# Optimization experiments

Hardware: AMD Instinct MI355X
Metric: run time of the kernel (lower is better)

The kernel has to match this reference:

```python
import jax, jax.numpy as jnp
import numpy as np

GROUP_MANTISSA = 8
GROUP_SIZE = 36


def bfp_quantize(x, mantissa=GROUP_MANTISSA, group_size=GROUP_SIZE):
    """Block floating point: flatten, group consecutive group_size elements,
    share the max exponent within each group, keep `mantissa` mantissa bits."""
    flat = x.reshape(-1)
    n = flat.shape[0]
    pad = (-n) % group_size
    f = jnp.pad(flat, (0, pad)).reshape(-1, group_size)  # [G, group_size]
    m = jnp.max(jnp.abs(f), axis=1, keepdims=True)       # group max magnitude
    safe_m = jnp.where(m > 0, m, jnp.ones_like(m))
    e = jnp.floor(jnp.log2(safe_m))                      # shared exponent
    scale = jnp.exp2(e - (mantissa - 1))                 # LSB step for the group
    q = jnp.round(f / scale) * scale
    q = jnp.where(m > 0, q, jnp.zeros_like(q))
    return q.reshape(-1)[:n].reshape(x.shape)


def setup_inputs() -> dict:
    key = jax.random.key(0)
    kx, kw, kb = jax.random.split(key, 3)
    x = jax.random.normal(kx, (32, 64, 112, 112), dtype=jnp.float32)
    # kaiming-uniform-ish scale for a 3x3x64 fan-in
    fan_in = 64 * 3 * 3
    bound = 1.0 / np.sqrt(fan_in)
    weight = jax.random.uniform(kw, (64, 64, 3, 3), dtype=jnp.float32, minval=-bound, maxval=bound) * np.sqrt(3.0)
    bias = jax.random.uniform(kb, (64,), dtype=jnp.float32, minval=-bound, maxval=bound)
    return {"x": x, "weight": weight, "bias": bias}


def reference(x, weight, bias):
    xq = bfp_quantize(x)
    wq = bfp_quantize(weight)
    out = jax.lax.conv_general_dilated(
        xq, wq,
        window_strides=(1, 1),
        padding=((1, 1), (1, 1)),
        lhs_dilation=(1, 1),
        rhs_dilation=(1, 1),
        dimension_numbers=("NCHW", "OIHW", "NCHW"),
        feature_group_count=1,
    )
    return out + bias[None, :, None, None]
```

## Files before the change

### kernel.cpp

```cpp
#include <hip/hip_runtime.h>

typedef __attribute__((ext_vector_type(4))) float f32x4;
typedef __attribute__((ext_vector_type(8))) short s16x8;
typedef __attribute__((ext_vector_type(2))) unsigned int u32x2;
typedef __attribute__((ext_vector_type(4))) unsigned int u32x4;

#define X_ELEMS 25690112
#define X_F4    6422528
#define HW 112
#define CHW (64*112*112)

__device__ __forceinline__ unsigned short f32_to_bf16_exact(float q) {
    return (unsigned short)(__float_as_uint(q) >> 16);
}

__device__ __forceinline__ unsigned int pack_bf16x2(float a, float b) {
    return __builtin_amdgcn_perm(__float_as_uint(b), __float_as_uint(a), 0x07060302u);
}

__device__ __forceinline__ void scale_from_max(float m, float& scale, float& inv) {
    if (m > 0.f) {
        int e = (int)((__float_as_uint(m) >> 23) & 0xFF) - 127;
        scale = __builtin_ldexpf(1.0f, e - 7);
        inv   = __builtin_ldexpf(1.0f, 7 - e);
    } else { scale = 0.f; inv = 0.f; }
}

__global__ __launch_bounds__(256) void q1_quant(const float* __restrict__ x,
                                                const float* __restrict__ w,
                                                unsigned short* __restrict__ xq,
                                                unsigned short* __restrict__ wt) {
    __shared__ float lmax[2304];
    __shared__ float lsc[256];
    __shared__ float linv[256];
    const int b = blockIdx.x, tid = threadIdx.x;

    if (b == 2788) {
        #pragma unroll 1
        for (int rep = 0; rep < 4; ++rep) {
            int g = rep * 256 + tid;
            const float4* p = (const float4*)w + g * 9;
            float vv[36]; float m = 0.f;
            #pragma unroll
            for (int i = 0; i < 9; ++i) {
                float4 v = p[i];
                vv[i*4+0]=v.x; vv[i*4+1]=v.y; vv[i*4+2]=v.z; vv[i*4+3]=v.w;
                m = fmaxf(m, fmaxf(fmaxf(fabsf(v.x), fabsf(v.y)), fmaxf(fabsf(v.z), fabsf(v.w))));
            }
            float s, inv; scale_from_max(m, s, inv);
            #pragma unroll
            for (int j = 0; j < 36; ++j) {
                int flat = g * 36 + j;
                int k = flat / 576, rem = flat % 576;
                int c = rem / 9, pp = rem % 9;
                float q = rintf(vv[j] * inv) * s;
                wt[pp * 4096 + k * 64 + c] = f32_to_bf16_exact(q);
            }
        }
        return;
    }

    long base4 = (long)b * 2304;
    float4 vv[9];
    #pragma unroll
    for (int it = 0; it < 9; ++it) {
        int i = it * 256 + tid;
        long g4 = base4 + i;
        float4 v = {0.f, 0.f, 0.f, 0.f};
        if (g4 < X_F4) v = ((const float4*)x)[g4];
        vv[it] = v;
        lmax[i] = fmaxf(fmaxf(fabsf(v.x), fabsf(v.y)), fmaxf(fabsf(v.z), fabsf(v.w)));
    }
    __syncthreads();
    {
        float m = 0.f; int o = tid * 9;
        #pragma unroll
        for (int j = 0; j < 9; ++j) m = fmaxf(m, lmax[o + j]);
        float s, inv; scale_from_max(m, s, inv);
        lsc[tid] = s; linv[tid] = inv;
    }
    __syncthreads();
    #pragma unroll
    for (int it = 0; it < 9; ++it) {
        int i = it * 256 + tid;
        long g4 = base4 + i;
        if (g4 < X_F4) {
            int lg = i / 9;
            float s = lsc[lg], inv = linv[lg];
            float4 v = vv[it];
            u32x2 o;
            o.x = pack_bf16x2(rintf(v.x * inv) * s, rintf(v.y * inv) * s);
            o.y = pack_bf16x2(rintf(v.z * inv) * s, rintf(v.w * inv) * s);
            *(u32x2*)(xq + g4 * 4) = o;
        }
    }
}

__device__ __forceinline__ int swz(int pix, int oct) {
    return pix * 72 + (((oct) ^ ((pix >> 3) & 7)) << 3);
}

__global__ __launch_bounds__(256, 2) void conv_mfma(const unsigned short* __restrict__ xq,
                                                    const unsigned short* __restrict__ wt,
                                                    const float* __restrict__ bias,
                                                    float* __restrict__ out) {
    __shared__ unsigned short xs[360 * 72];
    const int tid = threadIdx.x;
    const int wave = tid >> 6, lane = tid & 63;
    const int wl = lane & 15, quad = lane >> 4;
    const int kg = wave & 1, mg = wave >> 1;
    const int b = blockIdx.x;
    const int n = b / 56, rem = b % 56;
    const int h0 = (rem >> 2) * 8, w0 = (rem & 3) * 28;

    #pragma unroll
    for (int tt = 0; tt < 3; ++tt) {
        int t = tt * 256 + tid;
        if (t < 720) {
            int oct = t / 90;
            int rm = t - oct * 90;
            int r = rm / 9, i = rm - r * 9;
            int hh = h0 - 1 + r;
            int wb = w0 - 4 + i * 4;
            u32x2 v[8];
            if (hh >= 0 && hh < HW && wb >= 0 && wb <= 108) {
                const unsigned short* src = xq + ((n * 64 + oct * 8) * HW + hh) * HW + wb;
                #pragma unroll
                for (int j = 0; j < 8; ++j)
                    v[j] = *(const u32x2*)(src + j * 12544);
            } else {
                #pragma unroll
                for (int j = 0; j < 8; ++j) v[j] = (u32x2){0u, 0u};
            }
            int pix0 = r * 36 + i * 4;
            #pragma unroll
            for (int d = 0; d < 4; ++d) {
                unsigned int sel = (d & 1) ? 0x07060302u : 0x05040100u;
                u32x4 o;
                o.x = __builtin_amdgcn_perm(v[1][d >> 1], v[0][d >> 1], sel);
                o.y = __builtin_amdgcn_perm(v[3][d >> 1], v[2][d >> 1], sel);
                o.z = __builtin_amdgcn_perm(v[5][d >> 1], v[4][d >> 1], sel);
                o.w = __builtin_amdgcn_perm(v[7][d >> 1], v[6][d >> 1], sel);
                *(u32x4*)&xs[swz(pix0 + d, oct)] = o;
            }
        }
    }

    s16x8 Bf[9][2][2];
    #pragma unroll
    for (int p = 0; p < 9; ++p)
        #pragma unroll
        for (int cs = 0; cs < 2; ++cs)
            #pragma unroll
            for (int j = 0; j < 2; ++j)
                Bf[p][cs][j] = *(const s16x8*)(wt + p * 4096 +
                                ((kg * 2 + j) * 16 + wl) * 64 + cs * 32 + quad * 8);

    float bv[2];
    #pragma unroll
    for (int j = 0; j < 2; ++j) bv[j] = bias[kg * 32 + j * 16 + wl];

    int pixb[7], eofs[7];
    #pragma unroll
    for (int mti = 0; mti < 7; ++mti) {
        int m = (mg * 7 + mti) * 16 + wl;
        pixb[mti] = (m / 28) * 36 + (m % 28) + 3;
        int m0 = (mg * 7 + mti) * 16 + quad * 4;
        eofs[mti] = (m0 / 28) * HW + (m0 % 28);
    }

    __syncthreads();

    f32x4 acc[7][2];
    f32x4 zero = {0.f, 0.f, 0.f, 0.f};
    #pragma unroll
    for (int mti = 0; mti < 7; ++mti) { acc[mti][0] = zero; acc[mti][1] = zero; }

    #pragma unroll
    for (int p = 0; p < 9; ++p) {
        const int dpix = (p / 3) * 36 + (p % 3);
        #pragma unroll
        for (int mti = 0; mti < 7; ++mti) {
            int pix = pixb[mti] + dpix;
            #pragma unroll
            for (int cs = 0; cs < 2; ++cs) {
                s16x8 A = *(const s16x8*)&xs[swz(pix, cs * 4 + quad)];
                acc[mti][0] = __builtin_amdgcn_mfma_f32_16x16x32_bf16(A, Bf[p][cs][0], acc[mti][0], 0, 0, 0);
                acc[mti][1] = __builtin_amdgcn_mfma_f32_16x16x32_bf16(A, Bf[p][cs][1], acc[mti][1], 0, 0, 0);
            }
        }
    }

    int obase = n * CHW + h0 * HW + w0;
    #pragma unroll
    for (int mti = 0; mti < 7; ++mti) {
        #pragma unroll
        for (int j = 0; j < 2; ++j) {
            f32x4 v = acc[mti][j];
            v.x += bv[j]; v.y += bv[j]; v.z += bv[j]; v.w += bv[j];
            *(f32x4*)(out + obase + (kg * 32 + j * 16 + wl) * 12544 + eofs[mti]) = v;
        }
    }
}

extern "C" void kernel_launch(void* const* d_in, const int* in_sizes, int n_in,
                              void* d_out, int out_size, void* d_ws, size_t ws_size,
                              hipStream_t stream) {
    const float* x    = (const float*)d_in[0];
    const float* w    = (const float*)d_in[1];
    const float* bias = (const float*)d_in[2];
    float* out = (float*)d_out;
    char* ws = (char*)d_ws;
    unsigned short* xq = (unsigned short*)ws;
    unsigned short* wt = (unsigned short*)(ws + 51380224);

    hipLaunchKernelGGL(q1_quant,  dim3(2789), dim3(256), 0, stream, x, w, xq, wt);
    hipLaunchKernelGGL(conv_mfma, dim3(1792), dim3(256), 0, stream, xq, wt, bias, out);
}
```

Before: 277.5 us.

## Store quantized input in width-padded planes and load halo tiles with 16-byte reads

The quantize kernel now writes bf16 activations into planes padded to 116 columns, with zeroed border columns. This lets the conv kernel stage each halo row using 16-byte loads without per-chunk horizontal bounds checks, and with fewer staging threads. The conv kernel also remaps block indices to change the order in which tiles are scheduled, and raises its launch-bounds occupancy hint from 2 to 3. The cost is a larger workspace, extra index arithmetic and border-zero stores in the quantize kernel, and a possible register spill under the tighter occupancy target.

After: 301.8 us. 1.09x slower.

```diff
diff --git a/kernel.cpp b/kernel.cpp
--- a/kernel.cpp
+++ b/kernel.cpp
@@ -8,6 +8,8 @@
 #define X_ELEMS 25690112
 #define X_F4    6422528
 #define HW 112
+#define PW 116
+#define PPLANE (112*116)
 #define CHW (64*112*112)
 
 __device__ __forceinline__ unsigned short f32_to_bf16_exact(float q) {
@@ -83,7 +85,7 @@
     #pragma unroll
     for (int it = 0; it < 9; ++it) {
         int i = it * 256 + tid;
-        long g4 = base4 + i;
+        int g4 = (int)base4 + i;
         if (g4 < X_F4) {
             int lg = i / 9;
             float s = lsc[lg], inv = linv[lg];
@@ -91,7 +93,14 @@
             u32x2 o;
             o.x = pack_bf16x2(rintf(v.x * inv) * s, rintf(v.y * inv) * s);
             o.y = pack_bf16x2(rintf(v.z * inv) * s, rintf(v.w * inv) * s);
-            *(u32x2*)(xq + g4 * 4) = o;
+            int flat = g4 * 4;
+            int plane = flat / 12544;
+            int rw = flat - plane * 12544;
+            int h = rw / 112, ww = rw - h * 112;
+            int rowb = plane * PPLANE + h * PW;
+            *(u32x2*)(xq + rowb + 2 + ww) = o;
+            if (ww == 0)        *(unsigned int*)(xq + rowb) = 0u;
+            else if (ww == 108) *(unsigned int*)(xq + rowb + 114) = 0u;
         }
     }
 }
@@ -100,7 +109,7 @@
     return pix * 72 + (((oct) ^ ((pix >> 3) & 7)) << 3);
 }
 
-__global__ __launch_bounds__(256, 2) void conv_mfma(const unsigned short* __restrict__ xq,
+__global__ __launch_bounds__(256, 3) void conv_mfma(const unsigned short* __restrict__ xq,
                                                     const unsigned short* __restrict__ wt,
                                                     const float* __restrict__ bias,
                                                     float* __restrict__ out) {
@@ -109,38 +118,40 @@
     const int wave = tid >> 6, lane = tid & 63;
     const int wl = lane & 15, quad = lane >> 4;
     const int kg = wave & 1, mg = wave >> 1;
-    const int b = blockIdx.x;
+    int b = blockIdx.x;
+    b = (b & 7) * 224 + (b >> 3);
     const int n = b / 56, rem = b % 56;
     const int h0 = (rem >> 2) * 8, w0 = (rem & 3) * 28;
 
     #pragma unroll
-    for (int tt = 0; tt < 3; ++tt) {
+    for (int tt = 0; tt < 2; ++tt) {
         int t = tt * 256 + tid;
-        if (t < 720) {
-            int oct = t / 90;
-            int rm = t - oct * 90;
-            int r = rm / 9, i = rm - r * 9;
+        if (t < 320) {
+            int oct = t / 40;
+            int rm = t - oct * 40;
+            int r = rm >> 2, wq = rm & 3;
             int hh = h0 - 1 + r;
-            int wb = w0 - 4 + i * 4;
-            u32x2 v[8];
-            if (hh >= 0 && hh < HW && wb >= 0 && wb <= 108) {
-                const unsigned short* src = xq + ((n * 64 + oct * 8) * HW + hh) * HW + wb;
+            int c0 = w0 + wq * 8;
+            u32x4 v[8];
+            if (hh >= 0 && hh < HW) {
+                const unsigned short* src = xq + (n * 64 + oct * 8) * PPLANE + hh * PW + c0;
                 #pragma unroll
                 for (int j = 0; j < 8; ++j)
-                    v[j] = *(const u32x2*)(src + j * 12544);
+                    v[j] = *(const u32x4*)(src + j * PPLANE);
             } else {
                 #pragma unroll
-                for (int j = 0; j < 8; ++j) v[j] = (u32x2){0u, 0u};
-            }
-            int pix0 = r * 36 + i * 4;
-            #pragma unroll
-            for (int d = 0; d < 4; ++d) {
+                for (int j = 0; j < 8; ++j) v[j] = (u32x4){0u, 0u, 0u, 0u};
+            }
+            int pix0 = r * 36 + wq * 8 + 2;
+            #pragma unroll
+            for (int d = 0; d < 8; ++d) {
                 unsigned int sel = (d & 1) ? 0x07060302u : 0x05040100u;
+                int k = d >> 1;
                 u32x4 o;
-                o.x = __builtin_amdgcn_perm(v[1][d >> 1], v[0][d >> 1], sel);
-                o.y = __builtin_amdgcn_perm(v[3][d >> 1], v[2][d >> 1], sel);
-                o.z = __builtin_amdgcn_perm(v[5][d >> 1], v[4][d >> 1], sel);
-                o.w = __builtin_amdgcn_perm(v[7][d >> 1], v[6][d >> 1], sel);
+                o.x = __builtin_amdgcn_perm(v[1][k], v[0][k], sel);
+                o.y = __builtin_amdgcn_perm(v[3][k], v[2][k], sel);
+                o.z = __builtin_amdgcn_perm(v[5][k], v[4][k], sel);
+                o.w = __builtin_amdgcn_perm(v[7][k], v[6][k], sel);
                 *(u32x4*)&xs[swz(pix0 + d, oct)] = o;
             }
         }
@@ -212,7 +223,7 @@
     float* out = (float*)d_out;
     char* ws = (char*)d_ws;
     unsigned short* xq = (unsigned short*)ws;
-    unsigned short* wt = (unsigned short*)(ws + 51380224);
+    unsigned short* wt = (unsigned short*)(ws + 53215232);
 
     hipLaunchKernelGGL(q1_quant,  dim3(2789), dim3(256), 0, stream, x, w, xq, wt);
     hipLaunchKernelGGL(conv_mfma, dim3(1792), dim3(256), 0, stream, xq, wt, bias, out);
```
